# Optimization experiments

Measured on AMD Instinct MI355X. Metric: run time of the kernel, lower is better.

## Reference

```python
import jax, jax.numpy as jnp
import numpy as np

B, S, N_LM, MAX_LEN = 32, 384, 543, 384

_FACE = [33, 133, 362, 263, 61, 291, 199, 419, 17, 84, 314, 405, 320, 307, 375, 321, 308, 324, 318]
_SEL = np.array(_FACE + list(range(468, 489)) + list(range(522, 543)) + [11, 12, 13, 14, 15, 16], dtype=np.int32)  # 67 landmarks
# pairwise distance index pairs: i in range(3), j in i+1..min(i+3, L)
_PAIRS = [(0, 1), (0, 2), (1, 2), (1, 3), (2, 3), (2, 4)]


def setup_inputs() -> dict:
    key = jax.random.key(0)
    x = jax.random.normal(key, (B, S, N_LM, 3), dtype=jnp.float32)
    return {"x": x}


def _safe_norm(v):
    # torch.norm(v + 1e-8, dim=-1, keepdim=True)
    w = v + 1e-8
    return jnp.sqrt(jnp.sum(w * w, axis=-1, keepdims=True))


def reference(x):
    # select 67 landmarks, keep xy only (z never enters the feature stack)
    c = x[:, :, _SEL, :2]                                  # (B,S,67,2)
    # per-frame masked mean-centering (inputs are finite -> plain mean)
    c = c - jnp.mean(c, axis=2, keepdims=True)
    # per-frame std over flattened (L*2) values, unbiased (torch.std)
    bsz, seq, L, _ = c.shape
    std = jnp.std(c.reshape(bsz, seq, -1), axis=-1, ddof=1)  # (B,S)
    scale = jnp.where(std > 1e-6, 1.0 / std, 1.0)[:, :, None, None]
    c = c * scale                                          # (B,S,67,2)

    zrow = jnp.zeros((bsz, 1, L, 2), c.dtype)
    vel = jnp.concatenate([zrow, c[:, 1:] - c[:, :-1]], axis=1)
    acc = jnp.concatenate([jnp.zeros((bsz, 2, L, 2), c.dtype), vel[:, 2:] - vel[:, 1:-1]], axis=1)

    vm = _safe_norm(vel)                                   # (B,S,67,1)
    am = _safe_norm(acc)
    # cum[t] = sum_{k<t} vm[k]
    cum = jnp.concatenate([jnp.zeros((bsz, 1, L, 1), c.dtype), jnp.cumsum(vm[:, :-1], axis=1)], axis=1)

    ang = jnp.arctan2(vel[..., 1:2] + 1e-8, vel[..., 0:1] + 1e-8)
    dchg = jnp.concatenate([jnp.zeros((bsz, 2, L, 1), c.dtype), ang[:, 2:] - ang[:, 1:-1]], axis=1)

    dists = jnp.concatenate([_safe_norm(c[:, :, i] - c[:, :, j]) for i, j in _PAIRS], axis=-1)  # (B,S,6)

    flat = lambda a: a.reshape(bsz, seq, -1)
    feats = jnp.concatenate([flat(c), flat(vel), flat(acc), flat(vm), flat(am), flat(cum), flat(ang), flat(dchg), dists], axis=-1)
    feats = jnp.where(jnp.isfinite(feats), feats, 0.0)
    return feats[:, :MAX_LEN]
```

## Files before the change

kernel.cpp:

```cpp
#include <hip/hip_runtime.h>
#include <math.h>

#define NB 32
#define NS 384
#define NLM 543
#define NL 67
#define NF 743

__constant__ int d_SEL[NL] = {
    33, 133, 362, 263, 61, 291, 199, 419, 17, 84, 314, 405, 320, 307, 375, 321, 308, 324, 318,
    468, 469, 470, 471, 472, 473, 474, 475, 476, 477, 478, 479, 480, 481, 482, 483, 484, 485, 486, 487, 488,
    522, 523, 524, 525, 526, 527, 528, 529, 530, 531, 532, 533, 534, 535, 536, 537, 538, 539, 540, 541, 542,
    11, 12, 13, 14, 15, 16
};

__device__ __forceinline__ float fin(float v) { return isfinite(v) ? v : 0.0f; }


__device__ __forceinline__ void gather_norm(const float* __restrict__ xr,
                                            int o0, int o1, bool has1,
                                            float& c0x, float& c0y,
                                            float& c1x, float& c1y) {
    float a0x = xr[o0], a0y = xr[o0 + 1];
    float a1x = 0.f, a1y = 0.f;
    if (has1) { a1x = xr[o1]; a1y = xr[o1 + 1]; }

    float sx = a0x + a1x, sy = a0y + a1y;
    #pragma unroll
    for (int off = 32; off; off >>= 1) { sx += __shfl_xor(sx, off); sy += __shfl_xor(sy, off); }
    const float mx = sx * (1.0f / 67.0f), my = sy * (1.0f / 67.0f);

    c0x = a0x - mx; c0y = a0y - my;
    c1x = a1x - mx; c1y = a1y - my;

    float ss = c0x * c0x + c0y * c0y + (has1 ? (c1x * c1x + c1y * c1y) : 0.f);
    #pragma unroll
    for (int off = 32; off; off >>= 1) ss += __shfl_xor(ss, off);
    const float stdv = sqrtf(ss * (1.0f / 133.0f));
    const float scale = (stdv > 1e-6f) ? (1.0f / stdv) : 1.0f;

    c0x *= scale; c0y *= scale; c1x *= scale; c1y *= scale;
}

__global__ __launch_bounds__(256) void k_main(const float* __restrict__ x,
                                              float* __restrict__ out) {
    __shared__ float2 csh[6][NL];

    const int wave = threadIdx.x >> 6;
    const int lane = threadIdx.x & 63;
    const int b = blockIdx.x / 96;
    const int s_base = (blockIdx.x - b * 96) * 4;
    const int s = s_base + wave;
    const int bs = b * NS + s;

    const int lm0 = lane;
    const bool has1 = (lane < 3);
    const int lm1 = lane + 64;
    const int o0 = d_SEL[lm0] * 3;
    const int o1 = has1 ? d_SEL[lm1] * 3 : 0;

    const float* __restrict__ xb = x + (size_t)(b * NS) * (NLM * 3);

    float c0x, c0y, c1x, c1y;
    gather_norm(xb + (size_t)s * (NLM * 3), o0, o1, has1, c0x, c0y, c1x, c1y);
    csh[wave + 2][lm0] = make_float2(c0x, c0y);
    if (has1) csh[wave + 2][lm1] = make_float2(c1x, c1y);

    if (wave == 0) {
        if (s_base >= 1) {
            float bx, by, b1x, b1y;
            gather_norm(xb + (size_t)(s_base - 1) * (NLM * 3), o0, o1, has1, bx, by, b1x, b1y);
            csh[1][lm0] = make_float2(bx, by);
            if (has1) csh[1][lm1] = make_float2(b1x, b1y);
        } else {
            csh[1][lm0] = make_float2(0.f, 0.f);
            if (has1) csh[1][lm1] = make_float2(0.f, 0.f);
        }
    }
    if (wave == 1) {
        if (s_base >= 2) {
            float bx, by, b1x, b1y;
            gather_norm(xb + (size_t)(s_base - 2) * (NLM * 3), o0, o1, has1, bx, by, b1x, b1y);
            csh[0][lm0] = make_float2(bx, by);
            if (has1) csh[0][lm1] = make_float2(b1x, b1y);
        } else {
            csh[0][lm0] = make_float2(0.f, 0.f);
            if (has1) csh[0][lm1] = make_float2(0.f, 0.f);
        }
    }
    __syncthreads();

    float* __restrict__ row = out + (size_t)bs * NF;

    #pragma unroll
    for (int half = 0; half < 2; ++half) {
        if (half == 1 && !has1) break;
        const int lm = half ? lm1 : lm0;
        const float cx = half ? c1x : c0x, cy = half ? c1y : c0y;
        const float2 p = csh[wave + 1][lm];
        const float2 q = csh[wave][lm];

        const float vx = (s >= 1) ? (cx - p.x) : 0.f;
        const float vy = (s >= 1) ? (cy - p.y) : 0.f;
        const float v1x = p.x - q.x, v1y = p.y - q.y;
        const float ax = (s >= 2) ? (vx - v1x) : 0.f;
        const float ay = (s >= 2) ? (vy - v1y) : 0.f;

        const float wx = vx + 1e-8f, wy = vy + 1e-8f;
        const float vm = sqrtf(wx * wx + wy * wy);
        const float ux = ax + 1e-8f, uy = ay + 1e-8f;
        const float am = sqrtf(ux * ux + uy * uy);

        const float ang = atan2f(vy + 1e-8f, vx + 1e-8f);
        float dchg = 0.f;
        if (s >= 2) dchg = ang - atan2f(v1y + 1e-8f, v1x + 1e-8f);

        row[2 * lm]       = fin(cx);
        row[2 * lm + 1]   = fin(cy);
        row[134 + 2 * lm] = vx;
        row[135 + 2 * lm] = vy;
        row[268 + 2 * lm] = ax;
        row[269 + 2 * lm] = ay;
        row[402 + lm]     = vm;
        row[469 + lm]     = am;
        row[603 + lm]     = fin(ang);
        row[670 + lm]     = fin(dchg);
    }

    const int PI_[6] = {0, 0, 1, 1, 2, 2};
    const int PJ_[6] = {1, 2, 2, 3, 3, 4};
    const int p = (lane < 6) ? lane : 0;
    float xi = __shfl(c0x, PI_[p]); float yi = __shfl(c0y, PI_[p]);
    float xj = __shfl(c0x, PJ_[p]); float yj = __shfl(c0y, PJ_[p]);
    if (lane < 6) {
        float dx = xi - xj + 1e-8f, dy = yi - yj + 1e-8f;
        row[737 + lane] = fin(sqrtf(dx * dx + dy * dy));
    }
}

__global__ __launch_bounds__(128) void k_scan(float* __restrict__ out) {
    const int b = blockIdx.x;
    const int t = threadIdx.x;
    if (t >= NL) return;

    float acc = 0.f;
    #pragma unroll 8
    for (int s = 0; s < NS; ++s) {
        float* row = out + (size_t)(b * NS + s) * NF;
        row[536 + t] = fin(acc);
        acc += row[402 + t];
    }
}

extern "C" void kernel_launch(void* const* d_in, const int* in_sizes, int n_in,
                              void* d_out, int out_size, void* d_ws, size_t ws_size,
                              hipStream_t stream) {
    const float* x = (const float*)d_in[0];
    float* out = (float*)d_out;

    k_main<<<NB * (NS / 4), 256, 0, stream>>>(x, out);
    k_scan<<<NB, 128, 0, stream>>>(out);
}
```

Before: 153.9 us.

## Parallelize cumulative-sum scan with wave-level shuffles over transposed staging buffer

The main kernel now also writes velocity magnitudes into a workspace laid out as [batch][landmark][seq], so each sequence is contiguous. The scan kernel gives each (batch, landmark) pair its own 64-lane wave and computes the prefix sum with shuffle-up steps over six chunks, carrying the running total between chunks. This replaces the old serial 384-step loop per thread, which ran with only 32 blocks and strided reads of the output. It costs an extra scattered store per element in the main kernel and depends on the workspace being large enough.

```diff
diff --git a/kernel.cpp b/kernel.cpp
--- a/kernel.cpp
+++ b/kernel.cpp
@@ -43,7 +43,8 @@
 }
 
 __global__ __launch_bounds__(256) void k_main(const float* __restrict__ x,
-                                              float* __restrict__ out) {
+                                              float* __restrict__ out,
+                                              float* __restrict__ vmstage) {
     __shared__ float2 csh[6][NL];
 
     const int wave = threadIdx.x >> 6;
@@ -125,6 +126,7 @@
         row[469 + lm]     = am;
         row[603 + lm]     = fin(ang);
         row[670 + lm]     = fin(dchg);
+        vmstage[((size_t)b * NL + lm) * NS + s] = vm;
     }
 
     const int PI_[6] = {0, 0, 1, 1, 2, 2};
@@ -138,17 +140,27 @@
     }
 }
 
-__global__ __launch_bounds__(128) void k_scan(float* __restrict__ out) {
-    const int b = blockIdx.x;
-    const int t = threadIdx.x;
-    if (t >= NL) return;
+__global__ __launch_bounds__(256) void k_scan(const float* __restrict__ vmstage,
+                                              float* __restrict__ out) {
+    const int gw = (int)((blockIdx.x * 256u + threadIdx.x) >> 6);
+    const int lane = threadIdx.x & 63;
+    const int b = gw / NL;
+    const int lm = gw - b * NL;
+    const float* __restrict__ src = vmstage + (size_t)gw * NS;
 
-    float acc = 0.f;
-    #pragma unroll 8
-    for (int s = 0; s < NS; ++s) {
-        float* row = out + (size_t)(b * NS + s) * NF;
-        row[536 + t] = fin(acc);
-        acc += row[402 + t];
+    float carry = 0.f;
+    #pragma unroll
+    for (int k = 0; k < 6; ++k) {
+        const int t = k * 64 + lane;
+        const float v = src[t];
+        float incl = v;
+        #pragma unroll
+        for (int off = 1; off < 64; off <<= 1) {
+            float y = __shfl_up(incl, off);
+            if (lane >= off) incl += y;
+        }
+        out[((size_t)(b * NS + t)) * NF + 536 + lm] = fin(carry + (incl - v));
+        carry += __shfl(incl, 63);
     }
 }
 
@@ -157,7 +169,8 @@
                               hipStream_t stream) {
     const float* x = (const float*)d_in[0];
     float* out = (float*)d_out;
+    float* vmstage = (float*)d_ws;
 
-    k_main<<<NB * (NS / 4), 256, 0, stream>>>(x, out);
-    k_scan<<<NB, 128, 0, stream>>>(out);
+    k_main<<<NB * (NS / 4), 256, 0, stream>>>(x, out, vmstage);
+    k_scan<<<(NB * NL) / 4, 256, 0, stream>>>(vmstage, out);
 }
```

New measurement: 133.1 us. 1.16x faster.
